# Performance work log

Measured on AMD Instinct MI355X. Metric: run time of the kernel, lower is better.

Reference implementation:

```python
import jax, jax.numpy as jnp
import numpy as np

B = 16384
NUM_V = 1024
NUM_H = 1024
HYPER_DIM = 64
K = 10  # gibbs steps
T = 1.0


def setup_inputs() -> dict:
    key = jax.random.key(0)
    ks = jax.random.split(key, 9)
    v_data = jax.random.bernoulli(ks[0], 0.5, (B, NUM_V)).astype(jnp.float32)
    cond = jax.random.uniform(ks[1], (B, 1), jnp.float32)
    W = 0.01 * jax.random.normal(ks[2], (NUM_V, NUM_H), jnp.float32)
    b = 0.01 * jax.random.normal(ks[3], (NUM_V,), jnp.float32)
    c = 0.01 * jax.random.normal(ks[4], (NUM_H,), jnp.float32)
    fc1_w = jax.random.normal(ks[5], (HYPER_DIM, 1), jnp.float32)
    fc1_b = jnp.zeros((HYPER_DIM,), jnp.float32)
    fc2_w = jax.random.normal(ks[6], (2 * (NUM_V + NUM_H), HYPER_DIM), jnp.float32) / np.sqrt(HYPER_DIM)
    fc2_b = jnp.zeros((2 * (NUM_V + NUM_H),), jnp.float32)
    return {"v_data": v_data, "cond": cond, "W": W, "b": b, "c": c,
            "fc1_w": fc1_w, "fc1_b": fc1_b, "fc2_w": fc2_w, "fc2_b": fc2_b}


def _mod_biases(cond, b, c, fc1_w, fc1_b, fc2_w, fc2_b):
    x = jnp.tanh(cond @ fc1_w.T + fc1_b)
    y = x @ fc2_w.T + fc2_b  # [B, 2*(num_v+num_h)]
    gamma_b, beta_b, gamma_c, beta_c = jnp.split(
        y, [NUM_V, 2 * NUM_V, 2 * NUM_V + NUM_H], axis=-1)
    b_mod = (1.0 + gamma_b) * b[None, :] + beta_b  # [B, num_v]
    c_mod = (1.0 + gamma_c) * c[None, :] + beta_c  # [B, num_h]
    return b_mod, c_mod


def _free_energy(v, W, b_mod, c_mod):
    vW = v @ W  # [B, num_h]
    W_colsum = W.sum(axis=0)  # [num_h]
    sp_normal = jax.nn.softplus(vW + c_mod).sum(axis=-1)
    sp_flipped = jax.nn.softplus(W_colsum[None, :] - vW + c_mod).sum(axis=-1)
    vb_normal = -(v * b_mod).sum(axis=-1)
    vb_flipped = -((1.0 - v) * b_mod).sum(axis=-1)
    F_normal = vb_normal - sp_normal
    F_flipped = vb_flipped - sp_flipped
    negF = jnp.stack([-F_normal, -F_flipped], axis=-1)
    return -T * jax.nn.logsumexp(negF / T, axis=-1)


def _gibbs_step(carry, step_key, W, b_mod, c_mod):
    v, u = carry
    kh, ku, kv = jax.random.split(step_key, 3)
    v_branch = u * v + (1.0 - u) * (1.0 - v)
    p_h = jax.nn.sigmoid((v_branch @ W + c_mod) / T)
    h = jax.random.bernoulli(kh, p_h).astype(v.dtype)
    a = h @ W.T  # [B, num_v]
    dE = (-b_mod.sum(axis=-1) - a.sum(axis=-1)
          + 2.0 * (v * b_mod).sum(axis=-1) + 2.0 * (v * a).sum(axis=-1))
    p_u = jax.nn.sigmoid(dE / T)
    u = jax.random.bernoulli(ku, p_u).astype(v.dtype)[:, None]
    p_v = jax.nn.sigmoid((a + b_mod) / T)
    v_branch_new = jax.random.bernoulli(kv, p_v).astype(v.dtype)
    v_next = u * v_branch_new + (1.0 - u) * (1.0 - v_branch_new)
    return (v_next, u), None


def reference(v_data, cond, W, b, c, fc1_w, fc1_b, fc2_w, fc2_b):
    b_mod, c_mod = _mod_biases(cond, b, c, fc1_w, fc1_b, fc2_w, fc2_b)
    Bn = v_data.shape[0]
    key = jax.random.key(42)
    k_u, k_chain = jax.random.split(key)
    u0 = jax.random.bernoulli(k_u, 0.5, (Bn, 1)).astype(v_data.dtype)
    step_keys = jax.random.split(k_chain, K)
    step = lambda carry, sk: _gibbs_step(carry, sk, W, b_mod, c_mod)
    (v_model, _), _ = jax.lax.scan(step, (v_data, u0), step_keys)
    v_model = jax.lax.stop_gradient(v_model)
    loss = (_free_energy(v_data, W, b_mod, c_mod).mean()
            - _free_energy(v_model, W, b_mod, c_mod).mean())
    return loss
```

## Files before the change

### kernel.cpp

```cpp
#include <hip/hip_runtime.h>
#include <hip/hip_bf16.h>
#include <stdint.h>


#define NB 16384
#define KSTEPS 10
#define LDA 1152
#define KD 1088
#define NT 17
#define SLS 136
#define USALT 4000u
#define BONE ((unsigned char)7)
#define PSC 0x1.0p-13f
#define RWQ 1170.2857142857f
#define SGQ 64.0f
#define SXQ 128.0f

typedef __attribute__((ext_vector_type(4))) float f32x4;
typedef __attribute__((ext_vector_type(4))) int i32x4;
typedef __attribute__((ext_vector_type(4))) unsigned int u32x4;

__device__ __forceinline__ unsigned hash32(unsigned idx, unsigned salt) {
  unsigned x = idx + salt * 0x9E3779B9u;
  x = (x ^ (x >> 16)) * 0x7feb352du;
  x = (x ^ (x >> 15)) * 0x846ca68bu;
  return x ^ (x >> 16);
}
__device__ __forceinline__ float rng_u01(unsigned salt, unsigned idx) {
  return (float)(hash32(idx, salt) >> 8) * (1.0f / 16777216.0f);
}
__device__ __forceinline__ float sigm(float z) { return 1.0f / (1.0f + __expf(-z)); }
__device__ __forceinline__ float softplus_(float z) {
  return fmaxf(z, 0.f) + __logf(1.f + __expf(-fabsf(z)));
}
__device__ __forceinline__ float lse2(float a, float b) {
  float m = fmaxf(a, b);
  return m + log1pf(__expf(fminf(a, b) - m));
}
__device__ __forceinline__ unsigned char qi8(float v, float s) {
  float x = rintf(v * s);
  x = fminf(fmaxf(x, -127.f), 127.f);
  return (unsigned char)(signed char)(int)x;
}
__device__ __forceinline__ void gl2lds16(const void* g, void* l) {
  __builtin_amdgcn_global_load_lds(
      (const __attribute__((address_space(1))) unsigned int*)g,
      (__attribute__((address_space(3))) unsigned int*)l, 16, 0, 0);
}

template <int EPI>
__global__ __launch_bounds__(256, 4) void gemm_bt(
    const unsigned char* __restrict__ A, const unsigned char* __restrict__ Bt,
    unsigned char* sh, const float* __restrict__ cst,
    const float* __restrict__ wcs, const float* __restrict__ Xf,
    const float* __restrict__ pv0, const float* __restrict__ pv1, unsigned usalt,
    float* __restrict__ p0, float* __restrict__ p1, float* __restrict__ p2,
    unsigned salt) {
  constexpr int MI = (EPI == 2 ? 2 : 4);
  constexpr int BM = MI * 32;
  constexpr int ABYT = BM * 64;
  constexpr int BUF = ABYT + 8192;
  __shared__ __align__(16) char smem[2 * BUF];
  unsigned char* newsl = (unsigned char*)smem;

  const int t = threadIdx.x;
  const int L = blockIdx.x;
  const int xcd = L & 7, li = L >> 3;
  constexpr int MMSK = (EPI == 2 ? 31 : 15);
  constexpr int NSH = (EPI == 2 ? 5 : 4);
  const int m0 = xcd * 2048 + (li & MMSK) * BM;
  const int n0 = (li >> NSH) * 128;
  const int lane = t & 63, wave = t >> 6;
  const int wm = (wave >> 1) * (MI * 16), wn = (wave & 1) * 64;
  const int lr = lane & 15, quad = lane >> 4;
  const int row8 = lane >> 2;
  const int qch = (((lane & 3) ^ (row8 & 3) ^ ((lane >> 4) & 3)) << 4);
  const int rx = (lr & 3) ^ ((lr >> 2) & 3);
  const int kph = ((quad ^ rx) << 4);

  const unsigned char* gA0 = A + (size_t)(m0 + wave * (MI * 8) + row8) * LDA + qch;
  const unsigned char* gA1 = gA0 + (size_t)16 * LDA;
  const unsigned char* gB0 = Bt + (size_t)(n0 + wave * 32 + row8) * LDA + qch;
  const unsigned char* gB1 = gB0 + (size_t)16 * LDA;

  auto stage = [&](int it, int bufb) {
    const int ko = it * 64;
    if constexpr (EPI == 2) {
      gl2lds16(gA0 + ko, smem + bufb + wave * 1024);
    } else {
      gl2lds16(gA0 + ko, smem + bufb + wave * 2048);
      gl2lds16(gA1 + ko, smem + bufb + wave * 2048 + 1024);
    }
    gl2lds16(gB0 + ko, smem + bufb + ABYT + wave * 2048);
    gl2lds16(gB1 + ko, smem + bufb + ABYT + wave * 2048 + 1024);
  };

  i32x4 acc[MI][4] = {};
  i32x4 accf[EPI == 2 ? MI : 1][4] = {};

  stage(0, 0);
  __syncthreads();

#pragma unroll
  for (int it = 0; it < NT; ++it) {
    const int base = (it & 1) * BUF;
    if (it + 1 < NT) stage(it + 1, base ^ BUF);
    const char* sA = (const char*)smem + base;
    const char* sB = sA + ABYT;
    i32x4 af[MI], bfr[4];
#pragma unroll
    for (int i = 0; i < MI; i++)
      af[i] = *(const i32x4*)(sA + (wm + i * 16 + lr) * 64 + kph);
#pragma unroll
    for (int j = 0; j < 4; j++)
      bfr[j] = *(const i32x4*)(sB + (wn + j * 16 + lr) * 64 + kph);
    if (EPI == 2 && it >= 16) {
#pragma unroll
      for (int i = 0; i < MI; i++)
#pragma unroll
        for (int j = 0; j < 4; j++)
          accf[i][j] = __builtin_amdgcn_mfma_i32_16x16x64_i8(af[i], bfr[j], accf[i][j], 0, 0, 0);
    } else {
#pragma unroll
      for (int i = 0; i < MI; i++)
#pragma unroll
        for (int j = 0; j < 4; j++)
          acc[i][j] = __builtin_amdgcn_mfma_i32_16x16x64_i8(af[i], bfr[j], acc[i][j], 0, 0, 0);
    }
    __syncthreads();
  }

  float cst_j[4];
  if constexpr (EPI != 2) {
#pragma unroll
    for (int j = 0; j < 4; j++) cst_j[j] = cst[n0 + wn + j * 16 + lr];
  }

  if constexpr (EPI == 2) {
    if (n0 >= 1024) {
#pragma unroll
      for (int i = 0; i < MI; i++)
#pragma unroll
        for (int rg = 0; rg < 4; rg++) {
          const int r = m0 + wm + i * 16 + quad * 4 + rg;
          float pb = 0.f;
          if (wn == 0) {
#pragma unroll
            for (int j = 0; j < 4; j++)
              pb += (float)acc[i][j][rg] * Xf[(size_t)r * 64 + j * 16 + lr];
            pb *= (1.f / 448.f);
          } else {
            if (lr == 0) pb = (float)acc[i][0][rg] * PSC;
          }
#pragma unroll
          for (int msk = 1; msk < 16; msk <<= 1) pb += __shfl_xor(pb, msk, 64);
          if (lr == 0) atomicAdd(&p2[r], pb);
        }
      return;
    }
    float cstc_j[4];
#pragma unroll
    for (int j = 0; j < 4; j++) cstc_j[j] = cst[n0 + wn + j * 16 + lr];
#pragma unroll
    for (int i = 0; i < MI; i++)
#pragma unroll
      for (int rg = 0; rg < 4; rg++) {
        const int r = m0 + wm + i * 16 + quad * 4 + rg;
        bool uu = true;
        if (pv0 != nullptr) {
          const float dE = -pv0[r] + 2.f * pv1[r];
          uu = rng_u01(usalt, (unsigned)r) < sigm(dE);
        }
        float sn = 0.f, sf = 0.f;
#pragma unroll
        for (int j = 0; j < 4; j++) {
          const int n = n0 + wn + j * 16 + lr;
          const float vw = (float)acc[i][j][rg] * PSC;
          const float cm = (float)accf[i][j][rg] * PSC + cstc_j[j];
          const float s1 = softplus_(vw + cm);
          const float s2 = softplus_(wcs[n] - vw + cm);
          sn += uu ? s1 : s2;
          sf += uu ? s2 : s1;
        }
#pragma unroll
        for (int msk = 1; msk < 16; msk <<= 1) {
          sn += __shfl_xor(sn, msk, 64);
          sf += __shfl_xor(sf, msk, 64);
        }
        if (lr == 0) { atomicAdd(&p0[r], sn); atomicAdd(&p1[r], sf); }
      }
    return;
  }

  if constexpr (EPI == 1) {
    {
      const int rb = wave * (MI * 8);
#pragma unroll
      for (int q = 0; q < 4; ++q) {
        const int row = rb + q * 8 + (lane >> 3);
        const int sc = (lane & 7) ^ ((row >> 2) & 3);
        gl2lds16(sh + (size_t)(m0 + row) * LDA + n0 + sc * 16,
                 (unsigned char*)smem + BUF + (rb + q * 8) * 128);
      }
    }
    __syncthreads();
    const unsigned char* osl = (const unsigned char*)smem + BUF;
#pragma unroll
    for (int i = 0; i < MI; i++)
#pragma unroll
      for (int rg = 0; rg < 4; rg++) {
        const int r = m0 + wm + i * 16 + quad * 4 + rg;
        const int rowl = wm + i * 16 + quad * 4 + rg;
        const float dE = -pv0[r] + 2.f * pv1[r];
        const bool uu = rng_u01(usalt, (unsigned)r) < sigm(dE);
        float q0 = 0.f, q1 = 0.f;
#pragma unroll
        for (int j = 0; j < 4; ++j) {
          const float z = (float)acc[i][j][rg] * PSC + cst_j[j];
          const int pc = ((wn >> 4) + j) ^ quad;
          const float so = (osl[rowl * 128 + pc * 16 + lr] != 0) ? 1.f : 0.f;
          const float v = uu ? so : 1.f - so;
          q0 += z; q1 += v * z;
        }
#pragma unroll
        for (int msk = 1; msk < 16; msk <<= 1) {
          q0 += __shfl_xor(q0, msk, 64);
          q1 += __shfl_xor(q1, msk, 64);
        }
        if (lr == 0) { atomicAdd(&p0[r], q0); atomicAdd(&p1[r], q1); }
      }
    __syncthreads();
  }

#pragma unroll
  for (int i = 0; i < MI; ++i)
#pragma unroll
    for (int rg = 0; rg < 4; ++rg) {
      const int rowl = wm + i * 16 + quad * 4 + rg;
      const int r = m0 + rowl;
#pragma unroll
      for (int jp = 0; jp < 2; ++jp) {
        const unsigned x = hash32((unsigned)(r << 10) + (unsigned)(n0 + wn + jp * 16 + lr), salt);
        const float f0 = (float)(x & 0xFFFFu), f1 = (float)(x >> 16);
        const float z0 = (float)acc[i][jp][rg] * PSC + cst_j[jp];
        const float z1v = (float)acc[i][jp + 2][rg] * PSC + cst_j[jp + 2];
        newsl[rowl * SLS + wn + jp * 16 + lr] =
            (f0 * __expf(-z0) < 65536.f - f0) ? BONE : (unsigned char)0;
        newsl[rowl * SLS + wn + (jp + 2) * 16 + lr] =
            (f1 * __expf(-z1v) < 65536.f - f1) ? BONE : (unsigned char)0;
      }
    }
  __syncthreads();
#pragma unroll
  for (int p = 0; p < BM / 32; ++p) {
    const int c = p * 256 + t, rowl = c >> 3, chk = c & 7;
    const u32x4 vv = *(const u32x4*)(newsl + rowl * SLS + chk * 16);
    *(u32x4*)(sh + (size_t)(m0 + rowl) * LDA + n0 + chk * 16) = vv;
  }
}

__global__ __launch_bounds__(256) void k_x(const float* __restrict__ cond,
                                           const float* __restrict__ fc1w,
                                           const float* __restrict__ fc1b, float* __restrict__ X) {
  int idx = blockIdx.x * 256 + threadIdx.x;
  int r = idx >> 6, k = idx & 63;
  X[idx] = tanhf(cond[r] * fc1w[k] + fc1b[k]);
}

__global__ __launch_bounds__(256) void k_g(const float* __restrict__ fc2w,
                                           const float* __restrict__ fc2b,
                                           const float* __restrict__ b, const float* __restrict__ c,
                                           float* __restrict__ Gb, float* __restrict__ Gc,
                                           float* __restrict__ cstb, float* __restrict__ cstc) {
  int idx = blockIdx.x * 256 + threadIdx.x;
  int j = idx >> 6, k = idx & 63;
  Gb[idx] = fc2w[(size_t)j * 64 + k] * b[j] + fc2w[(size_t)(1024 + j) * 64 + k];
  Gc[idx] = fc2w[(size_t)(2048 + j) * 64 + k] * c[j] + fc2w[(size_t)(3072 + j) * 64 + k];
  if (k == 0) {
    cstb[j] = b[j] + fc2b[j] * b[j] + fc2b[1024 + j];
    cstc[j] = c[j] + fc2b[2048 + j] * c[j] + fc2b[3072 + j];
  }
}

__global__ __launch_bounds__(256) void k_prep(const float* __restrict__ W,
                                              const float* __restrict__ Gb,
                                              const float* __restrict__ Gc,
                                              const float* __restrict__ cstb,
                                              const float* __restrict__ cstc,
                                              unsigned char* __restrict__ Wt,
                                              unsigned char* __restrict__ Wb) {
  int k = blockIdx.x * 256 + threadIdx.x;
  int n = blockIdx.y;
  if (k >= LDA) return;
  unsigned char wt = 0, wb = 0;
  if (n < 1024) {
    if (k < 1024) {
      wt = qi8(W[(size_t)k * 1024 + n], RWQ);
      wb = qi8(W[(size_t)n * 1024 + k], RWQ);
    } else if (k < 1088) {
      int j = k - 1024;
      wt = qi8(Gc[(size_t)n * 64 + j], SGQ);
      wb = qi8(Gb[(size_t)n * 64 + j], SGQ);
    } else if (k == 1088) {
      wt = qi8(cstc[n], RWQ);
      wb = qi8(cstb[n], RWQ);
    }
  } else if (k < 1024) {
    if (n < 1088) wt = qi8(Gb[(size_t)k * 64 + (n - 1024)], SGQ);
    else if (n == 1088) wt = qi8(cstb[k], RWQ);
  }
  Wt[(size_t)n * LDA + k] = wt;
  Wb[(size_t)n * LDA + k] = wb;
}

__global__ __launch_bounds__(256) void k_wcs(const float* __restrict__ W, float* __restrict__ wcs) {
  int n = blockIdx.x * 256 + threadIdx.x;
  int i0 = blockIdx.y * 64;
  float s = 0.f;
  for (int i = i0; i < i0 + 64; i++) s += W[(size_t)i * 1024 + n];
  atomicAdd(&wcs[n], s);
}

__global__ __launch_bounds__(128) void k_aux(const float* __restrict__ Gb,
                                             const float* __restrict__ cstb,
                                             float* __restrict__ aux) {
  int t = threadIdx.x;
  if (t < 64) {
    float s = 0.f;
    for (int j = 0; j < 1024; j++) s += Gb[(size_t)j * 64 + t];
    aux[t] = s;
  } else if (t == 64) {
    float s = 0.f;
    for (int j = 0; j < 1024; j++) s += cstb[j];
    aux[64] = s;
  }
}

__global__ __launch_bounds__(256) void k_sinit(const float* __restrict__ vdata,
                                               const float* __restrict__ X,
                                               unsigned char* __restrict__ S,
                                               unsigned char* __restrict__ H,
                                               unsigned char* __restrict__ V) {
  const int idx = blockIdx.x * 256 + threadIdx.x;
  const int r = idx / 72, ch = idx - r * 72;
  const size_t o = (size_t)r * LDA + (size_t)ch * 16;
  union { u32x4 v4; unsigned char b[16]; } sv, vv;
  if (ch < 64) {
    const float4* vp = (const float4*)(vdata + (size_t)r * 1024 + ch * 16);
    const bool u0 = rng_u01(USALT, (unsigned)r) < 0.5f;
#pragma unroll
    for (int q = 0; q < 4; ++q) {
      const float4 f = vp[q];
      const float vs[4] = {f.x, f.y, f.z, f.w};
#pragma unroll
      for (int e = 0; e < 4; ++e) {
        const bool one = (vs[e] != 0.f);
        vv.b[q * 4 + e] = one ? BONE : (unsigned char)0;
        sv.b[q * 4 + e] = (u0 ? one : !one) ? BONE : (unsigned char)0;
      }
    }
    *(u32x4*)(V + o) = vv.v4;
    *(u32x4*)(S + o) = sv.v4;
  } else if (ch < 68) {
    const int j0 = (ch - 64) * 16;
#pragma unroll
    for (int e = 0; e < 16; ++e)
      sv.b[e] = qi8(X[(size_t)r * 64 + j0 + e], SXQ);
    *(u32x4*)(S + o) = sv.v4;
    *(u32x4*)(H + o) = sv.v4;
    *(u32x4*)(V + o) = sv.v4;
  } else {
    sv.v4 = (u32x4){0u, 0u, 0u, 0u};
    *(u32x4*)(S + o) = sv.v4;
    *(u32x4*)(H + o) = sv.v4;
    *(u32x4*)(V + o) = sv.v4;
  }
}

__global__ __launch_bounds__(256) void k_final(
    const float* __restrict__ Xf, const float* __restrict__ aux,
    const float* __restrict__ pv0, const float* __restrict__ pv1, unsigned usalt,
    const float* __restrict__ spn_d, const float* __restrict__ spf_d,
    const float* __restrict__ spn_m, const float* __restrict__ spf_m,
    const float* __restrict__ vb_d, const float* __restrict__ vb_m,
    float* __restrict__ fdiff) {
  __shared__ float ax[65];
  int t = threadIdx.x;
  if (t < 65) ax[t] = aux[t];
  __syncthreads();
  int r = blockIdx.x * 256 + t;
  float sb = ax[64];
  const float* xr = Xf + (size_t)r * 64;
#pragma unroll
  for (int k = 0; k < 64; k++) sb += xr[k] * ax[k];
  const float dE = -pv0[r] + 2.f * pv1[r];
  const bool uu = rng_u01(usalt, (unsigned)r) < sigm(dE);
  const float d1 = vb_d[r], d2 = vb_m[r];
  float F_d = -lse2(d1 + spn_d[r], (sb - d1) + spf_d[r]);
  float vbn = uu ? d2 : (sb - d2);
  float F_m = -lse2(vbn + spn_m[r], (sb - vbn) + spf_m[r]);
  fdiff[r] = F_d - F_m;
}

__global__ __launch_bounds__(256) void k_reduce(const float* __restrict__ fdiff,
                                                float* __restrict__ out) {
  __shared__ float red[4];
  int t = threadIdx.x;
  float s = 0.f;
  for (int i = t; i < NB; i += 256) s += fdiff[i];
  for (int m = 32; m >= 1; m >>= 1) s += __shfl_xor(s, m, 64);
  if ((t & 63) == 0) red[t >> 6] = s;
  __syncthreads();
  if (t == 0) out[0] = (red[0] + red[1] + red[2] + red[3]) * (1.0f / (float)NB);
}

extern "C" void kernel_launch(void* const* d_in, const int* in_sizes, int n_in, void* d_out,
                              int out_size, void* d_ws, size_t ws_size, hipStream_t stream) {
  const float* vdata = (const float*)d_in[0];
  const float* cond = (const float*)d_in[1];
  const float* W = (const float*)d_in[2];
  const float* bb = (const float*)d_in[3];
  const float* cc = (const float*)d_in[4];
  const float* fc1w = (const float*)d_in[5];
  const float* fc1b = (const float*)d_in[6];
  const float* fc2w = (const float*)d_in[7];
  const float* fc2b = (const float*)d_in[8];
  float* out = (float*)d_out;

  char* wp = (char*)d_ws;
  auto alloc = [&](size_t bytes) {
    char* p = wp;
    wp += (bytes + 255) & ~(size_t)255;
    return p;
  };
  unsigned char* Wt = (unsigned char*)alloc((size_t)1152 * LDA);
  unsigned char* Wb = (unsigned char*)alloc((size_t)1152 * LDA);
  float* wcs = (float*)alloc(1024 * 4);
  float* X = (float*)alloc((size_t)NB * 64 * 4);
  float* Gb = (float*)alloc((size_t)1024 * 64 * 4);
  float* Gc = (float*)alloc((size_t)1024 * 64 * 4);
  float* cstb = (float*)alloc(1024 * 4);
  float* cstc = (float*)alloc(1024 * 4);
  float* aux = (float*)alloc(65 * 4);
  unsigned char* S = (unsigned char*)alloc((size_t)NB * LDA);
  unsigned char* H = (unsigned char*)alloc((size_t)NB * LDA);
  unsigned char* V = (unsigned char*)alloc((size_t)NB * LDA);
  float* pall = (float*)alloc((size_t)(KSTEPS + 1 + 3) * 2 * NB * 4);
  float* spn_d = pall + (size_t)(KSTEPS + 1) * 2 * NB;
  float* spf_d = spn_d + NB;
  float* spn_m = spf_d + NB;
  float* spf_m = spn_m + NB;
  float* vb_d = spf_m + NB;
  float* vb_m = vb_d + NB;
  float* fdiff = (float*)alloc(NB * 4);
  auto P0 = [&](int t) { return pall + (size_t)(t + 1) * 2 * NB; };
  auto P1 = [&](int t) { return pall + (size_t)(t + 1) * 2 * NB + NB; };

  hipMemsetAsync(pall, 0, (size_t)(KSTEPS + 1 + 3) * 2 * NB * 4, stream);
  hipMemsetAsync(wcs, 0, 1024 * 4, stream);

  k_x<<<NB * 64 / 256, 256, 0, stream>>>(cond, fc1w, fc1b, X);
  k_g<<<1024 * 64 / 256, 256, 0, stream>>>(fc2w, fc2b, bb, cc, Gb, Gc, cstb, cstc);
  k_prep<<<dim3(5, 1152), 256, 0, stream>>>(W, Gb, Gc, cstb, cstc, Wt, Wb);
  k_wcs<<<dim3(4, 16), 256, 0, stream>>>(W, wcs);
  k_aux<<<1, 128, 0, stream>>>(Gb, cstb, aux);
  k_sinit<<<NB * 72 / 256, 256, 0, stream>>>(vdata, X, S, H, V);

  for (int step = 0; step < KSTEPS; ++step) {
    gemm_bt<0><<<1024, 256, 0, stream>>>(S, Wt, H, cstc, nullptr, nullptr,
                                         nullptr, nullptr, 0u, nullptr, nullptr, nullptr,
                                         2000u + (unsigned)step);
    gemm_bt<1><<<1024, 256, 0, stream>>>(H, Wb, S, cstb, nullptr, nullptr,
                                         P0(step - 1), P1(step - 1), USALT + (unsigned)step,
                                         P0(step), P1(step), nullptr,
                                         3000u + (unsigned)step);
  }

  gemm_bt<2><<<2304, 256, 0, stream>>>(V, Wt, nullptr, cstc, wcs, X, nullptr, nullptr, 0u,
                                       spn_d, spf_d, vb_d, 0u);
  gemm_bt<2><<<2304, 256, 0, stream>>>(S, Wt, nullptr, cstc, wcs, X,
                                       P0(KSTEPS - 1), P1(KSTEPS - 1), USALT + KSTEPS,
                                       spn_m, spf_m, vb_m, 0u);
  k_final<<<NB / 256, 256, 0, stream>>>(X, aux, P0(KSTEPS - 1), P1(KSTEPS - 1), USALT + KSTEPS,
                                        spn_d, spf_d, spn_m, spf_m, vb_d, vb_m, fdiff);
  k_reduce<<<1, 256, 0, stream>>>(fdiff, out);
}
```

Baseline: 944.2 us.

## Switch int8 GEMMs to single-wave 64x64 blocks with waitcnt-based pipelining

Each GEMM block is restructured from 4 waves on a 128x128 (or 64x128) tile to a single 64-lane wave on a 64x64 tile, with grids enlarged to match. All __syncthreads barriers are replaced by explicit s_waitcnt vmcnt/lgkmcnt waits on the async global-to-LDS loads. The old-sample tile prefetch for the step-1 epilogue is folded into the last main-loop iteration. This is meant to remove block-level barrier stalls and raise the number of resident blocks. The cost is less operand reuse per block: each wave now loads its own A and B tiles, which doubles global/L2 traffic per output.

```diff
diff --git a/kernel.cpp b/kernel.cpp
--- a/kernel.cpp
+++ b/kernel.cpp
@@ -8,7 +8,7 @@
 #define LDA 1152
 #define KD 1088
 #define NT 17
-#define SLS 136
+#define SLW 72
 #define USALT 4000u
 #define BONE ((unsigned char)7)
 #define PSC 0x1.0p-13f
@@ -49,102 +49,98 @@
 }
 
 template <int EPI>
-__global__ __launch_bounds__(256, 4) void gemm_bt(
+__global__ __launch_bounds__(64, EPI == 2 ? 2 : 3) void gemm_bt(
     const unsigned char* __restrict__ A, const unsigned char* __restrict__ Bt,
     unsigned char* sh, const float* __restrict__ cst,
     const float* __restrict__ wcs, const float* __restrict__ Xf,
     const float* __restrict__ pv0, const float* __restrict__ pv1, unsigned usalt,
     float* __restrict__ p0, float* __restrict__ p1, float* __restrict__ p2,
     unsigned salt) {
-  constexpr int MI = (EPI == 2 ? 2 : 4);
-  constexpr int BM = MI * 32;
-  constexpr int ABYT = BM * 64;
-  constexpr int BUF = ABYT + 8192;
-  __shared__ __align__(16) char smem[2 * BUF];
+  __shared__ __align__(16) char smem[16384];
   unsigned char* newsl = (unsigned char*)smem;
 
-  const int t = threadIdx.x;
+  const int lane = threadIdx.x;
   const int L = blockIdx.x;
   const int xcd = L & 7, li = L >> 3;
-  constexpr int MMSK = (EPI == 2 ? 31 : 15);
-  constexpr int NSH = (EPI == 2 ? 5 : 4);
-  const int m0 = xcd * 2048 + (li & MMSK) * BM;
-  const int n0 = (li >> NSH) * 128;
-  const int lane = t & 63, wave = t >> 6;
-  const int wm = (wave >> 1) * (MI * 16), wn = (wave & 1) * 64;
+  const int m0 = xcd * 2048 + (li & 31) * 64;
+  const int n0 = (li >> 5) * 64;
   const int lr = lane & 15, quad = lane >> 4;
   const int row8 = lane >> 2;
   const int qch = (((lane & 3) ^ (row8 & 3) ^ ((lane >> 4) & 3)) << 4);
   const int rx = (lr & 3) ^ ((lr >> 2) & 3);
   const int kph = ((quad ^ rx) << 4);
 
-  const unsigned char* gA0 = A + (size_t)(m0 + wave * (MI * 8) + row8) * LDA + qch;
-  const unsigned char* gA1 = gA0 + (size_t)16 * LDA;
-  const unsigned char* gB0 = Bt + (size_t)(n0 + wave * 32 + row8) * LDA + qch;
-  const unsigned char* gB1 = gB0 + (size_t)16 * LDA;
+  const unsigned char* gA = A + (size_t)(m0 + row8) * LDA + qch;
+  const unsigned char* gB = Bt + (size_t)(n0 + row8) * LDA + qch;
 
   auto stage = [&](int it, int bufb) {
     const int ko = it * 64;
-    if constexpr (EPI == 2) {
-      gl2lds16(gA0 + ko, smem + bufb + wave * 1024);
+#pragma unroll
+    for (int q = 0; q < 4; ++q) {
+      gl2lds16(gA + (size_t)q * 16 * LDA + ko, smem + bufb + q * 1024);
+      gl2lds16(gB + (size_t)q * 16 * LDA + ko, smem + bufb + 4096 + q * 1024);
+    }
+  };
+
+  i32x4 acc[4][4] = {};
+  i32x4 accf[EPI == 2 ? 4 : 1][4] = {};
+
+  stage(0, 0);
+
+#pragma unroll
+  for (int it = 0; it < NT; ++it) {
+    const int base = (it & 1) * 8192;
+    if (it + 1 < NT) {
+      asm volatile("s_waitcnt lgkmcnt(0)" ::: "memory");
+      stage(it + 1, base ^ 8192);
+      asm volatile("s_waitcnt vmcnt(8)" ::: "memory");
+    } else if (EPI == 1) {
+      asm volatile("s_waitcnt lgkmcnt(0)" ::: "memory");
+#pragma unroll
+      for (int q = 0; q < 4; ++q) {
+        const int row = q * 16 + row8;
+        const int sc = ((lane & 3) ^ ((row >> 2) & 3)) << 4;
+        gl2lds16(sh + (size_t)(m0 + row) * LDA + n0 + sc,
+                 (unsigned char*)smem + 8192 + q * 1024);
+      }
+      asm volatile("s_waitcnt vmcnt(4)" ::: "memory");
     } else {
-      gl2lds16(gA0 + ko, smem + bufb + wave * 2048);
-      gl2lds16(gA1 + ko, smem + bufb + wave * 2048 + 1024);
-    }
-    gl2lds16(gB0 + ko, smem + bufb + ABYT + wave * 2048);
-    gl2lds16(gB1 + ko, smem + bufb + ABYT + wave * 2048 + 1024);
-  };
-
-  i32x4 acc[MI][4] = {};
-  i32x4 accf[EPI == 2 ? MI : 1][4] = {};
-
-  stage(0, 0);
-  __syncthreads();
-
-#pragma unroll
-  for (int it = 0; it < NT; ++it) {
-    const int base = (it & 1) * BUF;
-    if (it + 1 < NT) stage(it + 1, base ^ BUF);
+      asm volatile("s_waitcnt vmcnt(0)" ::: "memory");
+    }
     const char* sA = (const char*)smem + base;
-    const char* sB = sA + ABYT;
-    i32x4 af[MI], bfr[4];
-#pragma unroll
-    for (int i = 0; i < MI; i++)
-      af[i] = *(const i32x4*)(sA + (wm + i * 16 + lr) * 64 + kph);
+    const char* sB = sA + 4096;
+    i32x4 af[4], bfr[4];
+#pragma unroll
+    for (int i = 0; i < 4; i++)
+      af[i] = *(const i32x4*)(sA + (i * 16 + lr) * 64 + kph);
 #pragma unroll
     for (int j = 0; j < 4; j++)
-      bfr[j] = *(const i32x4*)(sB + (wn + j * 16 + lr) * 64 + kph);
+      bfr[j] = *(const i32x4*)(sB + (j * 16 + lr) * 64 + kph);
     if (EPI == 2 && it >= 16) {
 #pragma unroll
-      for (int i = 0; i < MI; i++)
+      for (int i = 0; i < 4; i++)
 #pragma unroll
         for (int j = 0; j < 4; j++)
           accf[i][j] = __builtin_amdgcn_mfma_i32_16x16x64_i8(af[i], bfr[j], accf[i][j], 0, 0, 0);
     } else {
 #pragma unroll
-      for (int i = 0; i < MI; i++)
+      for (int i = 0; i < 4; i++)
 #pragma unroll
         for (int j = 0; j < 4; j++)
           acc[i][j] = __builtin_amdgcn_mfma_i32_16x16x64_i8(af[i], bfr[j], acc[i][j], 0, 0, 0);
     }
-    __syncthreads();
-  }
-
-  float cst_j[4];
-  if constexpr (EPI != 2) {
-#pragma unroll
-    for (int j = 0; j < 4; j++) cst_j[j] = cst[n0 + wn + j * 16 + lr];
-  }
+  }
+  if (EPI == 1) asm volatile("s_waitcnt vmcnt(0)" ::: "memory");
 
   if constexpr (EPI == 2) {
     if (n0 >= 1024) {
 #pragma unroll
-      for (int i = 0; i < MI; i++)
+      for (int i = 0; i < 4; i++)
 #pragma unroll
         for (int rg = 0; rg < 4; rg++) {
-          const int r = m0 + wm + i * 16 + quad * 4 + rg;
+          const int r = m0 + i * 16 + quad * 4 + rg;
           float pb = 0.f;
-          if (wn == 0) {
+          if (n0 == 1024) {
 #pragma unroll
             for (int j = 0; j < 4; j++)
               pb += (float)acc[i][j][rg] * Xf[(size_t)r * 64 + j * 16 + lr];
@@ -160,12 +156,12 @@
     }
     float cstc_j[4];
 #pragma unroll
-    for (int j = 0; j < 4; j++) cstc_j[j] = cst[n0 + wn + j * 16 + lr];
-#pragma unroll
-    for (int i = 0; i < MI; i++)
+    for (int j = 0; j < 4; j++) cstc_j[j] = cst[n0 + j * 16 + lr];
+#pragma unroll
+    for (int i = 0; i < 4; i++)
 #pragma unroll
       for (int rg = 0; rg < 4; rg++) {
-        const int r = m0 + wm + i * 16 + quad * 4 + rg;
+        const int r = m0 + i * 16 + quad * 4 + rg;
         bool uu = true;
         if (pv0 != nullptr) {
           const float dE = -pv0[r] + 2.f * pv1[r];
@@ -174,7 +170,7 @@
         float sn = 0.f, sf = 0.f;
 #pragma unroll
         for (int j = 0; j < 4; j++) {
-          const int n = n0 + wn + j * 16 + lr;
+          const int n = n0 + j * 16 + lr;
           const float vw = (float)acc[i][j][rg] * PSC;
           const float cm = (float)accf[i][j][rg] * PSC + cstc_j[j];
           const float s1 = softplus_(vw + cm);
@@ -192,33 +188,26 @@
     return;
   }
 
+  float cst_j[4];
+#pragma unroll
+  for (int j = 0; j < 4; j++) cst_j[j] = cst[n0 + j * 16 + lr];
+
   if constexpr (EPI == 1) {
-    {
-      const int rb = wave * (MI * 8);
-#pragma unroll
-      for (int q = 0; q < 4; ++q) {
-        const int row = rb + q * 8 + (lane >> 3);
-        const int sc = (lane & 7) ^ ((row >> 2) & 3);
-        gl2lds16(sh + (size_t)(m0 + row) * LDA + n0 + sc * 16,
-                 (unsigned char*)smem + BUF + (rb + q * 8) * 128);
-      }
-    }
-    __syncthreads();
-    const unsigned char* osl = (const unsigned char*)smem + BUF;
-#pragma unroll
-    for (int i = 0; i < MI; i++)
+    const unsigned char* osl = (const unsigned char*)smem + 8192;
+#pragma unroll
+    for (int i = 0; i < 4; i++)
 #pragma unroll
       for (int rg = 0; rg < 4; rg++) {
-        const int r = m0 + wm + i * 16 + quad * 4 + rg;
-        const int rowl = wm + i * 16 + quad * 4 + rg;
+        const int rowl = i * 16 + quad * 4 + rg;
+        const int r = m0 + rowl;
         const float dE = -pv0[r] + 2.f * pv1[r];
         const bool uu = rng_u01(usalt, (unsigned)r) < sigm(dE);
         float q0 = 0.f, q1 = 0.f;
 #pragma unroll
         for (int j = 0; j < 4; ++j) {
           const float z = (float)acc[i][j][rg] * PSC + cst_j[j];
-          const int pc = ((wn >> 4) + j) ^ quad;
-          const float so = (osl[rowl * 128 + pc * 16 + lr] != 0) ? 1.f : 0.f;
+          const int pc = (j ^ quad) << 4;
+          const float so = (osl[rowl * 64 + pc + lr] != 0) ? 1.f : 0.f;
           const float v = uu ? so : 1.f - so;
           q0 += z; q1 += v * z;
         }
@@ -229,32 +218,31 @@
         }
         if (lr == 0) { atomicAdd(&p0[r], q0); atomicAdd(&p1[r], q1); }
       }
-    __syncthreads();
-  }
-
-#pragma unroll
-  for (int i = 0; i < MI; ++i)
+  }
+
+#pragma unroll
+  for (int i = 0; i < 4; ++i)
 #pragma unroll
     for (int rg = 0; rg < 4; ++rg) {
-      const int rowl = wm + i * 16 + quad * 4 + rg;
+      const int rowl = i * 16 + quad * 4 + rg;
       const int r = m0 + rowl;
 #pragma unroll
       for (int jp = 0; jp < 2; ++jp) {
-        const unsigned x = hash32((unsigned)(r << 10) + (unsigned)(n0 + wn + jp * 16 + lr), salt);
+        const unsigned x = hash32((unsigned)(r << 10) + (unsigned)(n0 + jp * 16 + lr), salt);
         const float f0 = (float)(x & 0xFFFFu), f1 = (float)(x >> 16);
         const float z0 = (float)acc[i][jp][rg] * PSC + cst_j[jp];
         const float z1v = (float)acc[i][jp + 2][rg] * PSC + cst_j[jp + 2];
-        newsl[rowl * SLS + wn + jp * 16 + lr] =
+        newsl[rowl * SLW + jp * 16 + lr] =
             (f0 * __expf(-z0) < 65536.f - f0) ? BONE : (unsigned char)0;
-        newsl[rowl * SLS + wn + (jp + 2) * 16 + lr] =
+        newsl[rowl * SLW + (jp + 2) * 16 + lr] =
             (f1 * __expf(-z1v) < 65536.f - f1) ? BONE : (unsigned char)0;
       }
     }
-  __syncthreads();
-#pragma unroll
-  for (int p = 0; p < BM / 32; ++p) {
-    const int c = p * 256 + t, rowl = c >> 3, chk = c & 7;
-    const u32x4 vv = *(const u32x4*)(newsl + rowl * SLS + chk * 16);
+  asm volatile("s_waitcnt lgkmcnt(0)" ::: "memory");
+#pragma unroll
+  for (int p = 0; p < 4; ++p) {
+    const int c = p * 64 + lane, rowl = c >> 2, chk = c & 3;
+    const u32x4 vv = *(const u32x4*)(newsl + rowl * SLW + chk * 16);
     *(u32x4*)(sh + (size_t)(m0 + rowl) * LDA + n0 + chk * 16) = vv;
   }
 }
@@ -467,20 +455,20 @@
   k_sinit<<<NB * 72 / 256, 256, 0, stream>>>(vdata, X, S, H, V);
 
   for (int step = 0; step < KSTEPS; ++step) {
-    gemm_bt<0><<<1024, 256, 0, stream>>>(S, Wt, H, cstc, nullptr, nullptr,
-                                         nullptr, nullptr, 0u, nullptr, nullptr, nullptr,
-                                         2000u + (unsigned)step);
-    gemm_bt<1><<<1024, 256, 0, stream>>>(H, Wb, S, cstb, nullptr, nullptr,
-                                         P0(step - 1), P1(step - 1), USALT + (unsigned)step,
-                                         P0(step), P1(step), nullptr,
-                                         3000u + (unsigned)step);
-  }
-
-  gemm_bt<2><<<2304, 256, 0, stream>>>(V, Wt, nullptr, cstc, wcs, X, nullptr, nullptr, 0u,
-                                       spn_d, spf_d, vb_d, 0u);
-  gemm_bt<2><<<2304, 256, 0, stream>>>(S, Wt, nullptr, cstc, wcs, X,
-                                       P0(KSTEPS - 1), P1(KSTEPS - 1), USALT + KSTEPS,
-                                       spn_m, spf_m, vb_m, 0u);
+    gemm_bt<0><<<4096, 64, 0, stream>>>(S, Wt, H, cstc, nullptr, nullptr,
+                                        nullptr, nullptr, 0u, nullptr, nullptr, nullptr,
+                                        2000u + (unsigned)step);
+    gemm_bt<1><<<4096, 64, 0, stream>>>(H, Wb, S, cstb, nullptr, nullptr,
+                                        P0(step - 1), P1(step - 1), USALT + (unsigned)step,
+                                        P0(step), P1(step), nullptr,
+                                        3000u + (unsigned)step);
+  }
+
+  gemm_bt<2><<<4608, 64, 0, stream>>>(V, Wt, nullptr, cstc, wcs, X, nullptr, nullptr, 0u,
+                                      spn_d, spf_d, vb_d, 0u);
+  gemm_bt<2><<<4608, 64, 0, stream>>>(S, Wt, nullptr, cstc, wcs, X,
+                                      P0(KSTEPS - 1), P1(KSTEPS - 1), USALT + KSTEPS,
+                                      spn_m, spf_m, vb_m, 0u);
   k_final<<<NB / 256, 256, 0, stream>>>(X, aux, P0(KSTEPS - 1), P1(KSTEPS - 1), USALT + KSTEPS,
                                         spn_d, spf_d, spn_m, spf_m, vb_d, vb_m, fdiff);
   k_reduce<<<1, 256, 0, stream>>>(fdiff, out);
```

New measurement: 1.224 ms. +29.7%, slower.

## Tile-transpose W quantization and single-buffer the final free-energy GEMM

Applied to the files above, without the earlier changes.

Adds a tiled kernel that loads 64x64 blocks of W into shared memory and writes both the quantized W and its transpose with coalesced 16-byte stores. The old per-element prep kernel read W with strided accesses for the transpose, and it now skips that region. Separately, the EPI==2 GEMM variant drops double buffering in favour of one LDS buffer with load-then-compute per k step. This halves its shared memory, which may raise occupancy, but it loses the overlap of global loads with MFMA work.

```diff
diff --git a/kernel.cpp b/kernel.cpp
--- a/kernel.cpp
+++ b/kernel.cpp
@@ -60,7 +60,8 @@
   constexpr int BM = MI * 32;
   constexpr int ABYT = BM * 64;
   constexpr int BUF = ABYT + 8192;
-  __shared__ __align__(16) char smem[2 * BUF];
+  constexpr int NLDS = (EPI == 2 ? BUF : 2 * BUF);
+  __shared__ __align__(16) char smem[NLDS];
   unsigned char* newsl = (unsigned char*)smem;
 
   const int t = threadIdx.x;
@@ -98,36 +99,58 @@
   i32x4 acc[MI][4] = {};
   i32x4 accf[EPI == 2 ? MI : 1][4] = {};
 
-  stage(0, 0);
-  __syncthreads();
-
-#pragma unroll
-  for (int it = 0; it < NT; ++it) {
-    const int base = (it & 1) * BUF;
-    if (it + 1 < NT) stage(it + 1, base ^ BUF);
-    const char* sA = (const char*)smem + base;
-    const char* sB = sA + ABYT;
-    i32x4 af[MI], bfr[4];
-#pragma unroll
-    for (int i = 0; i < MI; i++)
-      af[i] = *(const i32x4*)(sA + (wm + i * 16 + lr) * 64 + kph);
-#pragma unroll
-    for (int j = 0; j < 4; j++)
-      bfr[j] = *(const i32x4*)(sB + (wn + j * 16 + lr) * 64 + kph);
-    if (EPI == 2 && it >= 16) {
+  if constexpr (EPI == 2) {
+#pragma unroll
+    for (int it = 0; it < NT; ++it) {
+      stage(it, 0);
+      __syncthreads();
+      const char* sA = (const char*)smem;
+      const char* sB = sA + ABYT;
+      i32x4 af[MI], bfr[4];
 #pragma unroll
       for (int i = 0; i < MI; i++)
-#pragma unroll
-        for (int j = 0; j < 4; j++)
-          accf[i][j] = __builtin_amdgcn_mfma_i32_16x16x64_i8(af[i], bfr[j], accf[i][j], 0, 0, 0);
-    } else {
+        af[i] = *(const i32x4*)(sA + (wm + i * 16 + lr) * 64 + kph);
+#pragma unroll
+      for (int j = 0; j < 4; j++)
+        bfr[j] = *(const i32x4*)(sB + (wn + j * 16 + lr) * 64 + kph);
+      if (it >= 16) {
+#pragma unroll
+        for (int i = 0; i < MI; i++)
+#pragma unroll
+          for (int j = 0; j < 4; j++)
+            accf[i][j] = __builtin_amdgcn_mfma_i32_16x16x64_i8(af[i], bfr[j], accf[i][j], 0, 0, 0);
+      } else {
+#pragma unroll
+        for (int i = 0; i < MI; i++)
+#pragma unroll
+          for (int j = 0; j < 4; j++)
+            acc[i][j] = __builtin_amdgcn_mfma_i32_16x16x64_i8(af[i], bfr[j], acc[i][j], 0, 0, 0);
+      }
+      __syncthreads();
+    }
+  } else {
+    stage(0, 0);
+    __syncthreads();
+#pragma unroll
+    for (int it = 0; it < NT; ++it) {
+      const int base = (it & 1) * BUF;
+      if (it + 1 < NT) stage(it + 1, base ^ BUF);
+      const char* sA = (const char*)smem + base;
+      const char* sB = sA + ABYT;
+      i32x4 af[MI], bfr[4];
+#pragma unroll
+      for (int i = 0; i < MI; i++)
+        af[i] = *(const i32x4*)(sA + (wm + i * 16 + lr) * 64 + kph);
+#pragma unroll
+      for (int j = 0; j < 4; j++)
+        bfr[j] = *(const i32x4*)(sB + (wn + j * 16 + lr) * 64 + kph);
 #pragma unroll
       for (int i = 0; i < MI; i++)
 #pragma unroll
         for (int j = 0; j < 4; j++)
           acc[i][j] = __builtin_amdgcn_mfma_i32_16x16x64_i8(af[i], bfr[j], acc[i][j], 0, 0, 0);
-    }
-    __syncthreads();
+      __syncthreads();
+    }
   }
 
   float cst_j[4];
@@ -282,6 +305,29 @@
   }
 }
 
+__global__ __launch_bounds__(256) void k_prepw(const float* __restrict__ W,
+                                               unsigned char* __restrict__ Wt,
+                                               unsigned char* __restrict__ Wb) {
+  __shared__ float tile[64][65];
+  const int t = threadIdx.x;
+  const int a0 = blockIdx.x * 64, b0 = blockIdx.y * 64;
+#pragma unroll
+  for (int e = 0; e < 16; ++e) {
+    const int idx = e * 256 + t;
+    tile[idx >> 6][idx & 63] = W[(size_t)(a0 + (idx >> 6)) * 1024 + b0 + (idx & 63)];
+  }
+  __syncthreads();
+  const int r = t >> 2, c = (t & 3) * 16;
+  union { u32x4 v4; unsigned char b[16]; } pb, pt;
+#pragma unroll
+  for (int e = 0; e < 16; ++e) {
+    pb.b[e] = qi8(tile[r][c + e], RWQ);
+    pt.b[e] = qi8(tile[c + e][r], RWQ);
+  }
+  *(u32x4*)(Wb + (size_t)(a0 + r) * LDA + b0 + c) = pb.v4;
+  *(u32x4*)(Wt + (size_t)(b0 + r) * LDA + a0 + c) = pt.v4;
+}
+
 __global__ __launch_bounds__(256) void k_prep(const float* __restrict__ W,
                                               const float* __restrict__ Gb,
                                               const float* __restrict__ Gc,
@@ -292,12 +338,10 @@
   int k = blockIdx.x * 256 + threadIdx.x;
   int n = blockIdx.y;
   if (k >= LDA) return;
+  if (n < 1024 && k < 1024) return;
   unsigned char wt = 0, wb = 0;
   if (n < 1024) {
-    if (k < 1024) {
-      wt = qi8(W[(size_t)k * 1024 + n], RWQ);
-      wb = qi8(W[(size_t)n * 1024 + k], RWQ);
-    } else if (k < 1088) {
+    if (k < 1088) {
       int j = k - 1024;
       wt = qi8(Gc[(size_t)n * 64 + j], SGQ);
       wb = qi8(Gb[(size_t)n * 64 + j], SGQ);
@@ -461,6 +505,7 @@
 
   k_x<<<NB * 64 / 256, 256, 0, stream>>>(cond, fc1w, fc1b, X);
   k_g<<<1024 * 64 / 256, 256, 0, stream>>>(fc2w, fc2b, bb, cc, Gb, Gc, cstb, cstc);
+  k_prepw<<<dim3(16, 16), 256, 0, stream>>>(W, Wt, Wb);
   k_prep<<<dim3(5, 1152), 256, 0, stream>>>(W, Gb, Gc, cstb, cstc, Wt, Wb);
   k_wcs<<<dim3(4, 16), 256, 0, stream>>>(W, wcs);
   k_aux<<<1, 128, 0, stream>>>(Gb, cstb, aux);
```

After: 951.6 us. Within noise of the previous version (+0.8%).
